# Optimization experiments

Hardware: AMD Instinct MI355X
Metric: run time of the kernel (lower is better)

The kernel has to match this reference:

```python
import jax, jax.numpy as jnp
import numpy as np

NUM_NODES = 512

def chebyshev_convolution(laplacian, signal, weights, t0):
    # Faithful port of the torch helper, including tk_prev staying equal to
    # `laplacian` throughout the loop (as in the source).
    k = weights.shape[0]
    # t0 is the identity, so t0 @ signal == signal
    out = jnp.matmul(signal, weights[0])
    out = out + jnp.matmul(jnp.matmul(laplacian, signal), weights[1])
    tk_prev = laplacian
    tk = 2.0 * jnp.matmul(laplacian, laplacian) - t0
    for i in range(2, k):
        out = out + jnp.matmul(jnp.matmul(tk, signal), weights[i])
        tk = 2.0 * jnp.matmul(laplacian, tk) - tk_prev
    return out


def setup_inputs() -> dict:
    key = jax.random.key(0)
    ks = jax.random.split(key, 5)
    B, T, N, C_IN, C_OUT, CS, CD = 4, 12, NUM_NODES, 64, 64, 3, 6
    std_l = 0.1 / np.sqrt(N)
    std_t = 0.1 / np.sqrt(C_IN)
    x = jax.random.normal(ks[0], (B, T, N, C_IN), dtype=jnp.float32)
    ws = jax.random.uniform(ks[1], (N, N), jnp.float32, -std_l, std_l)
    ts = jax.random.uniform(ks[2], (CS, C_IN, C_OUT), jnp.float32, -std_t, std_t)
    wp = jax.random.uniform(ks[3], (C_IN, C_IN), jnp.float32, -std_t, std_t)
    td = jax.random.uniform(ks[4], (CD, C_IN, C_OUT), jnp.float32, -std_t, std_t)
    return {"x": x, "ws": ws, "ts": ts, "wp": wp, "td": td}


def reference(x, ws, ts, wp, td):
    N = NUM_NODES
    t0 = jnp.eye(N, dtype=x.dtype)
    # Static (SGC) branch: Chebyshev conv with learned static Laplacian ws
    out_s = chebyshev_convolution(ws, x, ts, t0)
    # Dynamic branch: data-dependent Laplacian wd = x @ (wp @ x^T)  -> (B,T,N,N)
    wd = jnp.matmul(x, jnp.matmul(wp, jnp.swapaxes(x, -2, -1)))
    wd = wd + jnp.min(wd)
    wd = wd / jnp.max(wd) / (N ** 2)
    out_d = chebyshev_convolution(wd, x, td, t0)
    return out_s + out_d
```

## Files before the change

kernel.cpp:

```cpp
#include <hip/hip_runtime.h>
#include <cstddef>
#include <cstdint>

#define NN 512
#define CC 64
#define BT 48

typedef __bf16 bf16_t;
typedef bf16_t bf16x8 __attribute__((ext_vector_type(8)));
typedef bf16_t bf16x4 __attribute__((ext_vector_type(4)));
typedef float f32x4 __attribute__((ext_vector_type(4)));

#define OFF_MN    0
#define OFF_MX    384
#define OFF_WSB   1024
#define OFF_WS2B  132096
#define OFF_XBT   263168
#define OFF_XNB   1049600
#define OFF_XNR   1836032
#define OFF_CS0   2622464
#define OFF_T1T   2647040
#define OFF_T2T   2649088
#define OFF_Z1N   2651136
#define OFF_Z2N   3437568
#define OFF_WEB   4224000
#define OFF_WER   4322304
#define OFF_VDY   4420608

__device__ __forceinline__ f32x4 mfma(bf16x8 a, bf16x8 b, f32x4 c) {
  return __builtin_amdgcn_mfma_f32_16x16x32_bf16(a, b, c, 0, 0, 0);
}
__device__ __forceinline__ int swz_chunk(int r, int c8) {
  return r * 64 + ((c8 ^ (r & 7)) << 3);
}
__device__ __forceinline__ int swz_e(int r, int c) {
  return r * 64 + ((((c >> 3) ^ (r & 7)) << 3)) + (c & 7);
}
__device__ __forceinline__ bf16x8 frag(const bf16_t* sm, int row, int kc) {
  return *(const bf16x8*)(sm + row * 64 + ((kc ^ (row & 7)) << 3));
}
__device__ __forceinline__ void stage64(bf16_t* sm, const bf16_t* g, int ld, int tid) {
#pragma unroll
  for (int j = 0; j < 2; ++j) {
    int id = tid + 256 * j;
    int r = id >> 3, c8 = id & 7;
    bf16x8 v = *(const bf16x8*)(g + (size_t)r * ld + c8 * 8);
    *(bf16x8*)(sm + swz_chunk(r, c8)) = v;
  }
}
__device__ __forceinline__ void stage64f(bf16_t* sm, const float* g, int ld, int tid) {
#pragma unroll
  for (int j = 0; j < 4; ++j) {
    int idx = tid + 256 * j;
    int r = idx >> 4, cc = (idx & 15) * 4;
    float4 v = *(const float4*)(g + (size_t)r * ld + cc);
    bf16x4 o = {(bf16_t)v.x, (bf16_t)v.y, (bf16_t)v.z, (bf16_t)v.w};
    *(bf16x4*)(sm + swz_e(r, cc)) = o;
  }
}
struct bfpair { bf16_t b, r; };
__device__ __forceinline__ bfpair splitbf(float f) {
  bfpair p;
  p.b = (bf16_t)f;
  p.r = (bf16_t)(f - (float)p.b);
  return p;
}
__device__ __forceinline__ float dot16(const bf16_t* sm, int row, int sub,
                                       const float* vecF) {
  bf16x8 a0 = frag(sm, row, sub * 2);
  bf16x8 a1 = frag(sm, row, sub * 2 + 1);
  float s = 0.f;
#pragma unroll
  for (int q = 0; q < 8; ++q) {
    s += (float)a0[q] * vecF[sub * 16 + q];
    s += (float)a1[q] * vecF[sub * 16 + 8 + q];
  }
  return s;
}

__global__ __launch_bounds__(256) void k_pre(
    const float* __restrict__ x, const float* __restrict__ wsL,
    const float* __restrict__ ts, const float* __restrict__ wp,
    float* __restrict__ wsf)
{
  __shared__ __align__(16) char pool[32768];
  __shared__ float red[16];
  const int tid = threadIdx.x;
  const int b = blockIdx.x;
  const int w = tid >> 6, l = tid & 63, lh = l >> 4, lr = l & 15, m0 = w * 16;

  if (b < 384) {
    const int bt = (b & 7) + 8 * (b >> 6);
    const int it = (b >> 3) & 7;
    const int i0 = it * 64;
    float (*XsF)[66] = (float(*)[66])pool;
    bf16_t* XBT = (bf16_t*)(wsf + OFF_XBT);
    bf16_t* XNb = (bf16_t*)(wsf + OFF_XNB);
    bf16_t* XNr = (bf16_t*)(wsf + OFF_XNR);
    float* CS0 = wsf + OFF_CS0;
    const float* xg = x + ((size_t)bt * NN + i0) * CC;
    for (int j = 0; j < 4; ++j) {
      int idx = tid + 256 * j;
      int r = idx >> 4, c0v = (idx & 15) * 4;
      float4 v = *(const float4*)(xg + (size_t)r * CC + c0v);
      bfpair p0 = splitbf(v.x), p1 = splitbf(v.y), p2 = splitbf(v.z), p3 = splitbf(v.w);
      bf16x4 vb = {p0.b, p1.b, p2.b, p3.b};
      bf16x4 vr = {p0.r, p1.r, p2.r, p3.r};
      size_t gb = ((size_t)bt * 512 + i0 + r) * 64 + c0v;
      *(bf16x4*)(XNb + gb) = vb;
      *(bf16x4*)(XNr + gb) = vr;
      XsF[c0v + 0][r] = v.x; XsF[c0v + 1][r] = v.y;
      XsF[c0v + 2][r] = v.z; XsF[c0v + 3][r] = v.w;
    }
    __syncthreads();
    {
      int c = tid >> 2, k0 = (tid & 3) * 16;
      bf16x8 o1, o2;
#pragma unroll
      for (int q = 0; q < 8; ++q) {
        o1[q] = (bf16_t)XsF[c][k0 + q];
        o2[q] = (bf16_t)XsF[c][k0 + 8 + q];
      }
      size_t base = ((size_t)bt * 64 + c) * 512 + i0 + k0;
      *(bf16x8*)(XBT + base) = o1; *(bf16x8*)(XBT + base + 8) = o2;
    }
    if (tid < 64) {
      float s = 0.f;
      for (int r = 0; r < 64; ++r) s += XsF[tid][r];
      CS0[((size_t)bt * 8 + it) * 64 + tid] = s;
    }
    return;
  }
  if (b < 768) {
    const int g = b - 384;
    const int bt = (g & 7) + 8 * (g >> 6);
    const int bx = (g >> 3) & 7;
    bf16_t* WpT  = (bf16_t*)pool;
    bf16_t* Xa   = (bf16_t*)(pool + 8192);
    bf16_t* Hs   = (bf16_t*)(pool + 16384);
    bf16_t* Xcol = (bf16_t*)(pool + 24576);
    for (int j = 0; j < 4; ++j) {
      int idx = tid + 256 * j;
      int r = idx >> 4, cc = (idx & 15) * 4;
      float4 v = *(const float4*)(wp + r * 64 + cc);
      WpT[swz_e(cc + 0, r)] = (bf16_t)v.x;
      WpT[swz_e(cc + 1, r)] = (bf16_t)v.y;
      WpT[swz_e(cc + 2, r)] = (bf16_t)v.z;
      WpT[swz_e(cc + 3, r)] = (bf16_t)v.w;
    }
    stage64f(Xa, x + ((size_t)bt * NN + bx * 64) * CC, 64, tid);
    __syncthreads();
    f32x4 hacc[4] = {};
#pragma unroll
    for (int q = 0; q < 2; ++q) {
      bf16x8 a = frag(Xa, m0 + lr, q * 4 + lh);
#pragma unroll
      for (int t = 0; t < 4; ++t)
        hacc[t] = mfma(a, frag(WpT, t * 16 + lr, q * 4 + lh), hacc[t]);
    }
#pragma unroll
    for (int t = 0; t < 4; ++t)
#pragma unroll
      for (int r_ = 0; r_ < 4; ++r_)
        Hs[swz_e(m0 + 4 * lh + r_, t * 16 + lr)] = (bf16_t)hacc[t][r_];
    float mn = 3.4e38f, mx = -3.4e38f;
    for (int byj = 0; byj < 8; ++byj) {
      __syncthreads();
      stage64f(Xcol, x + ((size_t)bt * NN + byj * 64) * CC, 64, tid);
      __syncthreads();
      f32x4 acc[4] = {};
#pragma unroll
      for (int q = 0; q < 2; ++q) {
        bf16x8 a = frag(Hs, m0 + lr, q * 4 + lh);
#pragma unroll
        for (int t = 0; t < 4; ++t)
          acc[t] = mfma(a, frag(Xcol, t * 16 + lr, q * 4 + lh), acc[t]);
      }
#pragma unroll
      for (int t = 0; t < 4; ++t)
#pragma unroll
        for (int r_ = 0; r_ < 4; ++r_) {
          mn = fminf(mn, acc[t][r_]); mx = fmaxf(mx, acc[t][r_]);
        }
    }
    for (int off = 32; off; off >>= 1) {
      mn = fminf(mn, __shfl_xor(mn, off));
      mx = fmaxf(mx, __shfl_xor(mx, off));
    }
    if (l == 0) { red[w] = mn; red[8 + w] = mx; }
    __syncthreads();
    if (tid == 0) {
      mn = fminf(fminf(red[0], red[1]), fminf(red[2], red[3]));
      mx = fmaxf(fmaxf(red[8], red[9]), fmaxf(red[10], red[11]));
      wsf[OFF_MN + g] = mn; wsf[OFF_MX + g] = mx;
    }
    return;
  }
  if (b < 832) {
    const int idx2 = b - 768;
    bf16_t* Asb = (bf16_t*)pool;
    bf16_t* Bsb = (bf16_t*)(pool + 8192);
    bf16_t* Ys  = (bf16_t*)(pool + 16384);
    bf16_t* WS2B = (bf16_t*)(wsf + OFF_WS2B);
    const int r0 = (idx2 >> 3) * 64, c0 = (idx2 & 7) * 64;
    f32x4 acc[4] = {};
    for (int jj = 0; jj < 8; ++jj) {
      if (jj) __syncthreads();
      for (int j = 0; j < 4; ++j) {
        int idx = tid + 256 * j;
        int r = idx >> 4, cc = (idx & 15) * 4;
        float4 v = *(const float4*)(wsL + (size_t)(r0 + r) * 512 + jj * 64 + cc);
        bf16x4 vb = {(bf16_t)v.x, (bf16_t)v.y, (bf16_t)v.z, (bf16_t)v.w};
        *(bf16x4*)(Asb + swz_e(r, cc)) = vb;
        float4 u = *(const float4*)(wsL + (size_t)(jj * 64 + r) * 512 + c0 + cc);
        Bsb[swz_e(cc + 0, r)] = (bf16_t)u.x;
        Bsb[swz_e(cc + 1, r)] = (bf16_t)u.y;
        Bsb[swz_e(cc + 2, r)] = (bf16_t)u.z;
        Bsb[swz_e(cc + 3, r)] = (bf16_t)u.w;
      }
      __syncthreads();
#pragma unroll
      for (int q = 0; q < 2; ++q) {
        bf16x8 a = frag(Asb, m0 + lr, q * 4 + lh);
#pragma unroll
        for (int t = 0; t < 4; ++t)
          acc[t] = mfma(a, frag(Bsb, t * 16 + lr, q * 4 + lh), acc[t]);
      }
    }
#pragma unroll
    for (int t = 0; t < 4; ++t)
#pragma unroll
      for (int r_ = 0; r_ < 4; ++r_) {
        int row = m0 + 4 * lh + r_, col = t * 16 + lr;
        float v = 2.0f * acc[t][r_] - ((r0 + row) == (c0 + col) ? 1.0f : 0.0f);
        Ys[swz_e(row, col)] = (bf16_t)v;
      }
    __syncthreads();
#pragma unroll
    for (int j = 0; j < 2; ++j) {
      int id = tid + 256 * j;
      int r = id >> 3, c8 = id & 7;
      *(bf16x8*)(WS2B + (size_t)(r0 + r) * 512 + c0 + c8 * 8) =
          *(const bf16x8*)(Ys + swz_chunk(r, c8));
    }
    return;
  }
  if (b < 840) {
    const int bx = b - 832;
    const float* wrow = wsL + (size_t)bx * 64 * 512;
    bf16_t* wob = (bf16_t*)(wsf + OFF_WSB) + (size_t)bx * 64 * 512;
    for (int j = 0; j < 32; ++j) {
      int idx = tid + 256 * j;
      float4 v = *(const float4*)(wrow + (size_t)idx * 4);
      bf16x4 o = {(bf16_t)v.x, (bf16_t)v.y, (bf16_t)v.z, (bf16_t)v.w};
      *(bf16x4*)(wob + (size_t)idx * 4) = o;
    }
    return;
  }
  {
    bf16_t* T1 = (bf16_t*)(wsf + OFF_T1T);
    bf16_t* T2 = (bf16_t*)(wsf + OFF_T2T);
    const float* t1g = ts + 4096;
    const float* t2g = ts + 8192;
    for (int j = 0; j < 16; ++j) {
      int idx = tid + 256 * j;
      int cin = idx >> 6, co = idx & 63;
      T1[co * 64 + cin] = (bf16_t)t1g[cin * 64 + co];
      T2[co * 64 + cin] = (bf16_t)t2g[cin * 64 + co];
    }
  }
}

__global__ __launch_bounds__(256) void k_mix(
    const float* __restrict__ ts, const float* __restrict__ wp,
    const float* __restrict__ td, float* __restrict__ wsf)
{
  __shared__ __align__(16) char pool[66688];
  const int tid = threadIdx.x;
  const int bid = blockIdx.x;
  const int w = tid >> 6, l = tid & 63, lh = l >> 4, lr = l & 15, m0 = w * 16;

  if (bid >= 48) {
    const int g = bid - 48;
    const int bt = (g & 7) + 8 * (g >> 6);
    const int n0 = ((g >> 3) & 7) * 64;
    bf16_t* As = (bf16_t*)pool;
    bf16_t* B1 = (bf16_t*)(pool + 8192);
    bf16_t* B2 = (bf16_t*)(pool + 16384);
    const bf16_t* XBT = (const bf16_t*)(wsf + OFF_XBT);
    const bf16_t* WSB = (const bf16_t*)(wsf + OFF_WSB);
    const bf16_t* WS2B = (const bf16_t*)(wsf + OFF_WS2B);
    f32x4 acc1[4] = {}, acc2[4] = {};
    for (int kk = 0; kk < 8; ++kk) {
      if (kk) __syncthreads();
      stage64(As, XBT + (size_t)bt * 32768 + kk * 64, 512, tid);
      stage64(B1, WSB + (size_t)n0 * 512 + kk * 64, 512, tid);
      stage64(B2, WS2B + (size_t)n0 * 512 + kk * 64, 512, tid);
      __syncthreads();
#pragma unroll
      for (int q = 0; q < 2; ++q) {
        bf16x8 a = frag(As, m0 + lr, q * 4 + lh);
#pragma unroll
        for (int t = 0; t < 4; ++t) {
          acc1[t] = mfma(a, frag(B1, t * 16 + lr, q * 4 + lh), acc1[t]);
          acc2[t] = mfma(a, frag(B2, t * 16 + lr, q * 4 + lh), acc2[t]);
        }
      }
    }
    __syncthreads();
#pragma unroll
    for (int t = 0; t < 4; ++t)
#pragma unroll
      for (int r_ = 0; r_ < 4; ++r_) {
        int cy = m0 + 4 * lh + r_, nl = t * 16 + lr;
        As[swz_e(nl, cy)] = (bf16_t)acc1[t][r_];
        B1[swz_e(nl, cy)] = (bf16_t)acc2[t][r_];
      }
    __syncthreads();
    bf16_t* Z1N = (bf16_t*)(wsf + OFF_Z1N);
    bf16_t* Z2N = (bf16_t*)(wsf + OFF_Z2N);
#pragma unroll
    for (int j = 0; j < 2; ++j) {
      int id = tid + 256 * j;
      int r = id >> 3, c8 = id & 7;
      size_t gb = ((size_t)bt * 512 + n0 + r) * 64 + c8 * 8;
      *(bf16x8*)(Z1N + gb) = *(const bf16x8*)(As + swz_chunk(r, c8));
      *(bf16x8*)(Z2N + gb) = *(const bf16x8*)(B1 + swz_chunk(r, c8));
    }
    return;
  }
  const int bt = bid;
  bf16_t* XB  = (bf16_t*)pool;
  bf16_t* Ab0 = (bf16_t*)pool;
  bf16_t* AT0 = (bf16_t*)(pool + 8192);
  bf16_t* Ab1 = (bf16_t*)(pool + 16384);
  bf16_t* AT1 = (bf16_t*)(pool + 24576);
  bf16_t* Gb  = (bf16_t*)(pool + 32768);
  bf16_t* WpT = (bf16_t*)(pool + 40960);
  bf16_t* tdA = (bf16_t*)(pool + 49152);
  bf16_t* tdB = (bf16_t*)(pool + 57344);
  float* vec = (float*)(pool + 65536);
  float* uF = vec;        float* hF = vec + 64;
  float* b0 = vec + 128;  float* b1 = vec + 192;
  float* redv = vec + 256;
  const bf16_t* XBTg = (const bf16_t*)(wsf + OFF_XBT);
  const float* CS0 = wsf + OFF_CS0;
  for (int kk = 0; kk < 8; ++kk)
    stage64(XB + kk * 4096, XBTg + (size_t)bt * 32768 + kk * 64, 512, tid);
  {
    float mn = 3.4e38f, mx = -3.4e38f;
    for (int i = tid; i < 384; i += 256) {
      mn = fminf(mn, wsf[OFF_MN + i]);
      mx = fmaxf(mx, wsf[OFF_MX + i]);
    }
    for (int off = 32; off; off >>= 1) {
      mn = fminf(mn, __shfl_xor(mn, off));
      mx = fmaxf(mx, __shfl_xor(mx, off));
    }
    if (l == 0) { redv[w] = mn; redv[8 + w] = mx; }
  }
  if (tid < 64) {
    float s = 0.f;
#pragma unroll
    for (int p = 0; p < 8; ++p) s += CS0[((size_t)bt * 8 + p) * 64 + tid];
    uF[tid] = s; b0[tid] = s;
  }
  __syncthreads();
  f32x4 pacc[4] = {};
  for (int kk = 0; kk < 8; ++kk) {
    const bf16_t* xt = XB + kk * 4096;
#pragma unroll
    for (int q = 0; q < 2; ++q) {
      bf16x8 a = frag(xt, m0 + lr, q * 4 + lh);
#pragma unroll
      for (int t = 0; t < 4; ++t)
        pacc[t] = mfma(a, frag(xt, t * 16 + lr, q * 4 + lh), pacc[t]);
    }
  }
  const float mnA = fminf(fminf(redv[0], redv[1]), fminf(redv[2], redv[3]));
  const float mxA = fmaxf(fmaxf(redv[8], redv[9]), fmaxf(redv[10], redv[11]));
  const float s_sc = 1.0f / (mxA + mnA) / 262144.0f;
  const float c_sc = mnA * s_sc;
  __syncthreads();
#pragma unroll
  for (int t = 0; t < 4; ++t)
#pragma unroll
    for (int r_ = 0; r_ < 4; ++r_) {
      int m = m0 + 4 * lh + r_, jc = t * 16 + lr;
      bf16_t bv = (bf16_t)pacc[t][r_];
      Ab0[swz_e(m, jc)] = bv; AT0[swz_e(jc, m)] = bv;
    }
  for (int j = 0; j < 4; ++j) {
    int idx = tid + 256 * j;
    int r = idx >> 4, cc = (idx & 15) * 4;
    float4 v = *(const float4*)(wp + r * 64 + cc);
    WpT[swz_e(cc + 0, r)] = (bf16_t)v.x;
    WpT[swz_e(cc + 1, r)] = (bf16_t)v.y;
    WpT[swz_e(cc + 2, r)] = (bf16_t)v.z;
    WpT[swz_e(cc + 3, r)] = (bf16_t)v.w;
  }
  for (int j = 0; j < 4; ++j) {
    int idx = tid + 256 * j;
    int cin = idx >> 4, co = (idx & 15) * 4;
    float4 v = *(const float4*)(td + 4096 + cin * 64 + co);
    tdA[swz_e(co + 0, cin)] = (bf16_t)v.x;
    tdA[swz_e(co + 1, cin)] = (bf16_t)v.y;
    tdA[swz_e(co + 2, cin)] = (bf16_t)v.z;
    tdA[swz_e(co + 3, cin)] = (bf16_t)v.w;
  }
  __syncthreads();
  {
    int jj = tid >> 2, sub = tid & 3;
    float s = dot16(WpT, jj, sub, uF);
    s += __shfl_xor(s, 1); s += __shfl_xor(s, 2);
    if (sub == 0) hF[jj] = s;
  }
  {
    f32x4 gv[4] = {};
#pragma unroll
    for (int q = 0; q < 2; ++q) {
      bf16x8 a = frag(Ab0, m0 + lr, q * 4 + lh);
#pragma unroll
      for (int t = 0; t < 4; ++t)
        gv[t] = mfma(a, frag(WpT, t * 16 + lr, q * 4 + lh), gv[t]);
    }
#pragma unroll
    for (int t = 0; t < 4; ++t)
#pragma unroll
      for (int r_ = 0; r_ < 4; ++r_)
        Gb[swz_e(m0 + 4 * lh + r_, t * 16 + lr)] = (bf16_t)gv[t][r_];
  }
  __syncthreads();
  float mu = 0.f, vacc = 0.f;
  f32x4 Macc[4] = {};
  for (int i = 1; i <= 5; ++i) {
    const float* bcur = (i & 1) ? b0 : b1;
    float* bnx = (i & 1) ? b1 : b0;
    const bf16_t* tdc = (i & 1) ? tdA : tdB;
    const bf16_t* AbC = (i & 1) ? Ab0 : Ab1;
    const bf16_t* ATC = (i & 1) ? AT0 : AT1;
    bf16_t* AbN = (i & 1) ? Ab1 : Ab0;
    bf16_t* ATN = (i & 1) ? AT1 : AT0;
    if (i < 5) {
      bf16_t* tdn = (i & 1) ? tdB : tdA;
      for (int j = 0; j < 4; ++j) {
        int idx = tid + 256 * j;
        int cin = idx >> 4, co = (idx & 15) * 4;
        float4 v = *(const float4*)(td + (i + 1) * 4096 + cin * 64 + co);
        tdn[swz_e(co + 0, cin)] = (bf16_t)v.x;
        tdn[swz_e(co + 1, cin)] = (bf16_t)v.y;
        tdn[swz_e(co + 2, cin)] = (bf16_t)v.z;
        tdn[swz_e(co + 3, cin)] = (bf16_t)v.w;
      }
    }
#pragma unroll
    for (int q = 0; q < 2; ++q) {
      bf16x8 a = frag(AbC, m0 + lr, q * 4 + lh);
#pragma unroll
      for (int t = 0; t < 4; ++t)
        Macc[t] = mfma(a, frag(tdc, t * 16 + lr, q * 4 + lh), Macc[t]);
    }
    f32x4 Aacc[4] = {};
    if (i < 5) {
#pragma unroll
      for (int q = 0; q < 2; ++q) {
        bf16x8 gfr = frag(Gb, m0 + lr, q * 4 + lh);
#pragma unroll
        for (int t = 0; t < 4; ++t)
          Aacc[t] = mfma(gfr, frag(ATC, t * 16 + lr, q * 4 + lh), Aacc[t]);
      }
    }
    {
      int co = tid >> 2, sub = tid & 3;
      float sv = dot16(tdc, co, sub, bcur);
      sv += __shfl_xor(sv, 1); sv += __shfl_xor(sv, 2);
      if (sub == 0) vacc += sv;
    }
    if (i < 5) {
      int jj = tid >> 2, sub = tid & 3;
      float t1 = dot16(ATC, jj, sub, hF);
      t1 += __shfl_xor(t1, 1); t1 += __shfl_xor(t1, 2);
      if (sub == 0)
        bnx[jj] = 2.f * (s_sc * t1 + 512.f * c_sc * bcur[jj] + mu * uF[jj])
                  - (i >= 2 ? uF[jj] : 0.f);
    }
    if (i < 5) {
#pragma unroll
      for (int t = 0; t < 4; ++t)
#pragma unroll
        for (int r_ = 0; r_ < 4; ++r_) {
          int m = m0 + 4 * lh + r_, jc = t * 16 + lr;
          float v = 2.f * (s_sc * Aacc[t][r_] + c_sc * uF[m] * bcur[jc] + mu * pacc[t][r_])
                    - (i >= 2 ? pacc[t][r_] : 0.f);
          bf16_t bv = (bf16_t)v;
          AbN[swz_e(m, jc)] = bv; ATN[swz_e(jc, m)] = bv;
        }
      mu = (i == 1) ? -1.f : 0.f;
    }
    __syncthreads();
  }
  bf16_t* Mst = tdA;
  bf16_t* WpN = tdB;
#pragma unroll
  for (int t = 0; t < 4; ++t)
#pragma unroll
    for (int r_ = 0; r_ < 4; ++r_)
      Mst[swz_e(t * 16 + lr, m0 + 4 * lh + r_)] = (bf16_t)Macc[t][r_];
  for (int j = 0; j < 4; ++j) {
    int idx = tid + 256 * j;
    int r = idx >> 4, cc = (idx & 15) * 4;
    float4 v = *(const float4*)(wp + r * 64 + cc);
    bf16x4 o = {(bf16_t)v.x, (bf16_t)v.y, (bf16_t)v.z, (bf16_t)v.w};
    *(bf16x4*)(WpN + swz_e(r, cc)) = o;
  }
  __syncthreads();
  f32x4 wm[4] = {};
#pragma unroll
  for (int q = 0; q < 2; ++q) {
    bf16x8 a = frag(WpN, m0 + lr, q * 4 + lh);
#pragma unroll
    for (int t = 0; t < 4; ++t)
      wm[t] = mfma(a, frag(Mst, t * 16 + lr, q * 4 + lh), wm[t]);
  }
  bf16_t* WEb = (bf16_t*)(wsf + OFF_WEB);
  bf16_t* WEr = (bf16_t*)(wsf + OFF_WER);
#pragma unroll
  for (int t = 0; t < 4; ++t)
#pragma unroll
    for (int r_ = 0; r_ < 4; ++r_) {
      int a_ = m0 + 4 * lh + r_, co = t * 16 + lr;
      float weff = ts[a_ * 64 + co] + td[a_ * 64 + co] - td[2 * 4096 + a_ * 64 + co]
                   + s_sc * wm[t][r_];
      bfpair p = splitbf(weff);
      WEb[((size_t)bt * 64 + co) * 64 + a_] = p.b;
      WEr[((size_t)bt * 64 + co) * 64 + a_] = p.r;
    }
  if ((tid & 3) == 0) (wsf + OFF_VDY)[bt * 64 + (tid >> 2)] = c_sc * vacc;
}

__global__ __launch_bounds__(256) void k_epi(float* __restrict__ wsf,
                                             float* __restrict__ out)
{
  __shared__ __align__(16) bf16_t Xb[4096], Xr[4096], Z1s[4096], Z2s[4096],
                                  WEs[4096], WRs[4096], T1s[4096], T2s[4096];
  const int tid = threadIdx.x;
  const int g = blockIdx.x;
  const int bt = (g & 7) + 8 * (g >> 6);
  const int n0 = ((g >> 3) & 7) * 64;
  const int w = tid >> 6, l = tid & 63, lh = l >> 4, lr = l & 15, m0 = w * 16;
  stage64(Xb,  (const bf16_t*)(wsf + OFF_XNB) + ((size_t)bt * 512 + n0) * 64, 64, tid);
  stage64(Xr,  (const bf16_t*)(wsf + OFF_XNR) + ((size_t)bt * 512 + n0) * 64, 64, tid);
  stage64(Z1s, (const bf16_t*)(wsf + OFF_Z1N) + ((size_t)bt * 512 + n0) * 64, 64, tid);
  stage64(Z2s, (const bf16_t*)(wsf + OFF_Z2N) + ((size_t)bt * 512 + n0) * 64, 64, tid);
  stage64(WEs, (const bf16_t*)(wsf + OFF_WEB) + (size_t)bt * 4096, 64, tid);
  stage64(WRs, (const bf16_t*)(wsf + OFF_WER) + (size_t)bt * 4096, 64, tid);
  stage64(T1s, (const bf16_t*)(wsf + OFF_T1T), 64, tid);
  stage64(T2s, (const bf16_t*)(wsf + OFF_T2T), 64, tid);
  __syncthreads();
  const float* VDY = wsf + OFF_VDY;
  f32x4 accO[4];
#pragma unroll
  for (int t = 0; t < 4; ++t) {
    float vv = VDY[bt * 64 + t * 16 + lr];
    accO[t] = {vv, vv, vv, vv};
  }
#pragma unroll
  for (int q = 0; q < 2; ++q) {
    bf16x8 aXb = frag(Xb, m0 + lr, q * 4 + lh);
    bf16x8 aXr = frag(Xr, m0 + lr, q * 4 + lh);
    bf16x8 aZ1 = frag(Z1s, m0 + lr, q * 4 + lh);
    bf16x8 aZ2 = frag(Z2s, m0 + lr, q * 4 + lh);
#pragma unroll
    for (int t = 0; t < 4; ++t) {
      bf16x8 bWb = frag(WEs, t * 16 + lr, q * 4 + lh);
      bf16x8 bWr = frag(WRs, t * 16 + lr, q * 4 + lh);
      accO[t] = mfma(aXb, bWb, accO[t]);
      accO[t] = mfma(aXb, bWr, accO[t]);
      accO[t] = mfma(aXr, bWb, accO[t]);
      accO[t] = mfma(aZ1, frag(T1s, t * 16 + lr, q * 4 + lh), accO[t]);
      accO[t] = mfma(aZ2, frag(T2s, t * 16 + lr, q * 4 + lh), accO[t]);
    }
  }
#pragma unroll
  for (int t = 0; t < 4; ++t)
#pragma unroll
    for (int r_ = 0; r_ < 4; ++r_)
      out[((size_t)bt * 512 + n0 + m0 + 4 * lh + r_) * 64 + t * 16 + lr] = accO[t][r_];
}

extern "C" void kernel_launch(void* const* d_in, const int* in_sizes, int n_in,
                              void* d_out, int out_size, void* d_ws, size_t ws_size,
                              hipStream_t stream)
{
  (void)in_sizes; (void)n_in; (void)out_size; (void)ws_size;
  const float* x   = (const float*)d_in[0];
  const float* wsL = (const float*)d_in[1];
  const float* ts  = (const float*)d_in[2];
  const float* wp  = (const float*)d_in[3];
  const float* td  = (const float*)d_in[4];
  float* out = (float*)d_out;
  float* wsf = (float*)d_ws;
  dim3 b(256);

  k_pre<<<841, b, 0, stream>>>(x, wsL, ts, wp, wsf);
  k_mix<<<432, b, 0, stream>>>(ts, wp, td, wsf);
  k_epi<<<384, b, 0, stream>>>(wsf, out);
}
```

Before: 43.47 us.

## Split dynamic min/max blocks in half and shrink k_mix shared memory

Measured after the change: 44.98 us. +3.5%, slower.

```diff
diff --git a/kernel.cpp b/kernel.cpp
--- a/kernel.cpp
+++ b/kernel.cpp
@@ -12,20 +12,20 @@
 typedef float f32x4 __attribute__((ext_vector_type(4)));
 
 #define OFF_MN    0
-#define OFF_MX    384
-#define OFF_WSB   1024
-#define OFF_WS2B  132096
-#define OFF_XBT   263168
-#define OFF_XNB   1049600
-#define OFF_XNR   1836032
-#define OFF_CS0   2622464
-#define OFF_T1T   2647040
-#define OFF_T2T   2649088
-#define OFF_Z1N   2651136
-#define OFF_Z2N   3437568
-#define OFF_WEB   4224000
-#define OFF_WER   4322304
-#define OFF_VDY   4420608
+#define OFF_MX    768
+#define OFF_WSB   2048
+#define OFF_WS2B  133120
+#define OFF_XBT   264192
+#define OFF_XNB   1050624
+#define OFF_XNR   1837056
+#define OFF_CS0   2623488
+#define OFF_T1T   2648064
+#define OFF_T2T   2650112
+#define OFF_Z1N   2652160
+#define OFF_Z2N   3438592
+#define OFF_WEB   4225024
+#define OFF_WER   4323328
+#define OFF_VDY   4421632
 
 __device__ __forceinline__ f32x4 mfma(bf16x8 a, bf16x8 b, f32x4 c) {
   return __builtin_amdgcn_mfma_f32_16x16x32_bf16(a, b, c, 0, 0, 0);
@@ -131,10 +131,12 @@
     }
     return;
   }
-  if (b < 768) {
+  if (b < 1152) {
     const int g = b - 384;
-    const int bt = (g & 7) + 8 * (g >> 6);
-    const int bx = (g >> 3) & 7;
+    const int gg = (g >= 384) ? g - 384 : g;
+    const int half = (g >= 384) ? 1 : 0;
+    const int bt = (gg & 7) + 8 * (gg >> 6);
+    const int bx = (gg >> 3) & 7;
     bf16_t* WpT  = (bf16_t*)pool;
     bf16_t* Xa   = (bf16_t*)(pool + 8192);
     bf16_t* Hs   = (bf16_t*)(pool + 16384);
@@ -164,7 +166,7 @@
       for (int r_ = 0; r_ < 4; ++r_)
         Hs[swz_e(m0 + 4 * lh + r_, t * 16 + lr)] = (bf16_t)hacc[t][r_];
     float mn = 3.4e38f, mx = -3.4e38f;
-    for (int byj = 0; byj < 8; ++byj) {
+    for (int byj = half * 4; byj < half * 4 + 4; ++byj) {
       __syncthreads();
       stage64f(Xcol, x + ((size_t)bt * NN + byj * 64) * CC, 64, tid);
       __syncthreads();
@@ -196,8 +198,8 @@
     }
     return;
   }
-  if (b < 832) {
-    const int idx2 = b - 768;
+  if (b < 1216) {
+    const int idx2 = b - 1152;
     bf16_t* Asb = (bf16_t*)pool;
     bf16_t* Bsb = (bf16_t*)(pool + 8192);
     bf16_t* Ys  = (bf16_t*)(pool + 16384);
@@ -245,8 +247,8 @@
     }
     return;
   }
-  if (b < 840) {
-    const int bx = b - 832;
+  if (b < 1224) {
+    const int bx = b - 1216;
     const float* wrow = wsL + (size_t)bx * 64 * 512;
     bf16_t* wob = (bf16_t*)(wsf + OFF_WSB) + (size_t)bx * 64 * 512;
     for (int j = 0; j < 32; ++j) {
@@ -275,7 +277,7 @@
     const float* __restrict__ ts, const float* __restrict__ wp,
     const float* __restrict__ td, float* __restrict__ wsf)
 {
-  __shared__ __align__(16) char pool[66688];
+  __shared__ __align__(16) char pool[50240];
   const int tid = threadIdx.x;
   const int bid = blockIdx.x;
   const int w = tid >> 6, l = tid & 63, lh = l >> 4, lr = l & 15, m0 = w * 16;
@@ -330,51 +332,53 @@
     return;
   }
   const int bt = bid;
-  bf16_t* XB  = (bf16_t*)pool;
-  bf16_t* Ab0 = (bf16_t*)pool;
-  bf16_t* AT0 = (bf16_t*)(pool + 8192);
-  bf16_t* Ab1 = (bf16_t*)(pool + 16384);
-  bf16_t* AT1 = (bf16_t*)(pool + 24576);
-  bf16_t* Gb  = (bf16_t*)(pool + 32768);
-  bf16_t* WpT = (bf16_t*)(pool + 40960);
-  bf16_t* tdA = (bf16_t*)(pool + 49152);
-  bf16_t* tdB = (bf16_t*)(pool + 57344);
-  float* vec = (float*)(pool + 65536);
+  bf16_t* XB   = (bf16_t*)pool;
+  bf16_t* Ab0  = (bf16_t*)pool;
+  bf16_t* AT0  = (bf16_t*)(pool + 8192);
+  bf16_t* Ab1  = (bf16_t*)(pool + 16384);
+  bf16_t* AT1  = (bf16_t*)(pool + 24576);
+  bf16_t* Gb   = (bf16_t*)(pool + 32768);
+  bf16_t* WpTD = (bf16_t*)(pool + 40960);
+  float* vec = (float*)(pool + 49152);
   float* uF = vec;        float* hF = vec + 64;
   float* b0 = vec + 128;  float* b1 = vec + 192;
   float* redv = vec + 256;
   const bf16_t* XBTg = (const bf16_t*)(wsf + OFF_XBT);
   const float* CS0 = wsf + OFF_CS0;
-  for (int kk = 0; kk < 8; ++kk)
-    stage64(XB + kk * 4096, XBTg + (size_t)bt * 32768 + kk * 64, 512, tid);
-  {
-    float mn = 3.4e38f, mx = -3.4e38f;
-    for (int i = tid; i < 384; i += 256) {
-      mn = fminf(mn, wsf[OFF_MN + i]);
-      mx = fmaxf(mx, wsf[OFF_MX + i]);
-    }
-    for (int off = 32; off; off >>= 1) {
-      mn = fminf(mn, __shfl_xor(mn, off));
-      mx = fmaxf(mx, __shfl_xor(mx, off));
-    }
-    if (l == 0) { redv[w] = mn; redv[8 + w] = mx; }
-  }
-  if (tid < 64) {
-    float s = 0.f;
-#pragma unroll
-    for (int p = 0; p < 8; ++p) s += CS0[((size_t)bt * 8 + p) * 64 + tid];
-    uF[tid] = s; b0[tid] = s;
-  }
-  __syncthreads();
   f32x4 pacc[4] = {};
-  for (int kk = 0; kk < 8; ++kk) {
-    const bf16_t* xt = XB + kk * 4096;
-#pragma unroll
-    for (int q = 0; q < 2; ++q) {
-      bf16x8 a = frag(xt, m0 + lr, q * 4 + lh);
-#pragma unroll
-      for (int t = 0; t < 4; ++t)
-        pacc[t] = mfma(a, frag(xt, t * 16 + lr, q * 4 + lh), pacc[t]);
+  for (int pass = 0; pass < 2; ++pass) {
+    if (pass) __syncthreads();
+    for (int kk = 0; kk < 4; ++kk)
+      stage64(XB + kk * 4096,
+              XBTg + (size_t)bt * 32768 + (pass * 4 + kk) * 64, 512, tid);
+    if (pass == 0) {
+      float mn = 3.4e38f, mx = -3.4e38f;
+      for (int i = tid; i < 768; i += 256) {
+        mn = fminf(mn, wsf[OFF_MN + i]);
+        mx = fmaxf(mx, wsf[OFF_MX + i]);
+      }
+      for (int off = 32; off; off >>= 1) {
+        mn = fminf(mn, __shfl_xor(mn, off));
+        mx = fmaxf(mx, __shfl_xor(mx, off));
+      }
+      if (l == 0) { redv[w] = mn; redv[8 + w] = mx; }
+      if (tid < 64) {
+        float s = 0.f;
+#pragma unroll
+        for (int p = 0; p < 8; ++p) s += CS0[((size_t)bt * 8 + p) * 64 + tid];
+        uF[tid] = s; b0[tid] = s;
+      }
+    }
+    __syncthreads();
+    for (int kk = 0; kk < 4; ++kk) {
+      const bf16_t* xt = XB + kk * 4096;
+#pragma unroll
+      for (int q = 0; q < 2; ++q) {
+        bf16x8 a = frag(xt, m0 + lr, q * 4 + lh);
+#pragma unroll
+        for (int t = 0; t < 4; ++t)
+          pacc[t] = mfma(a, frag(xt, t * 16 + lr, q * 4 + lh), pacc[t]);
+      }
     }
   }
   const float mnA = fminf(fminf(redv[0], redv[1]), fminf(redv[2], redv[3]));
@@ -394,41 +398,42 @@
     int idx = tid + 256 * j;
     int r = idx >> 4, cc = (idx & 15) * 4;
     float4 v = *(const float4*)(wp + r * 64 + cc);
-    WpT[swz_e(cc + 0, r)] = (bf16_t)v.x;
-    WpT[swz_e(cc + 1, r)] = (bf16_t)v.y;
-    WpT[swz_e(cc + 2, r)] = (bf16_t)v.z;
-    WpT[swz_e(cc + 3, r)] = (bf16_t)v.w;
-  }
+    WpTD[swz_e(cc + 0, r)] = (bf16_t)v.x;
+    WpTD[swz_e(cc + 1, r)] = (bf16_t)v.y;
+    WpTD[swz_e(cc + 2, r)] = (bf16_t)v.z;
+    WpTD[swz_e(cc + 3, r)] = (bf16_t)v.w;
+  }
+  __syncthreads();
+  {
+    int jj = tid >> 2, sub = tid & 3;
+    float s = dot16(WpTD, jj, sub, uF);
+    s += __shfl_xor(s, 1); s += __shfl_xor(s, 2);
+    if (sub == 0) hF[jj] = s;
+  }
+  {
+    f32x4 gv[4] = {};
+#pragma unroll
+    for (int q = 0; q < 2; ++q) {
+      bf16x8 a = frag(Ab0, m0 + lr, q * 4 + lh);
+#pragma unroll
+      for (int t = 0; t < 4; ++t)
+        gv[t] = mfma(a, frag(WpTD, t * 16 + lr, q * 4 + lh), gv[t]);
+    }
+#pragma unroll
+    for (int t = 0; t < 4; ++t)
+#pragma unroll
+      for (int r_ = 0; r_ < 4; ++r_)
+        Gb[swz_e(m0 + 4 * lh + r_, t * 16 + lr)] = (bf16_t)gv[t][r_];
+  }
+  __syncthreads();
   for (int j = 0; j < 4; ++j) {
     int idx = tid + 256 * j;
     int cin = idx >> 4, co = (idx & 15) * 4;
     float4 v = *(const float4*)(td + 4096 + cin * 64 + co);
-    tdA[swz_e(co + 0, cin)] = (bf16_t)v.x;
-    tdA[swz_e(co + 1, cin)] = (bf16_t)v.y;
-    tdA[swz_e(co + 2, cin)] = (bf16_t)v.z;
-    tdA[swz_e(co + 3, cin)] = (bf16_t)v.w;
-  }
-  __syncthreads();
-  {
-    int jj = tid >> 2, sub = tid & 3;
-    float s = dot16(WpT, jj, sub, uF);
-    s += __shfl_xor(s, 1); s += __shfl_xor(s, 2);
-    if (sub == 0) hF[jj] = s;
-  }
-  {
-    f32x4 gv[4] = {};
-#pragma unroll
-    for (int q = 0; q < 2; ++q) {
-      bf16x8 a = frag(Ab0, m0 + lr, q * 4 + lh);
-#pragma unroll
-      for (int t = 0; t < 4; ++t)
-        gv[t] = mfma(a, frag(WpT, t * 16 + lr, q * 4 + lh), gv[t]);
-    }
-#pragma unroll
-    for (int t = 0; t < 4; ++t)
-#pragma unroll
-      for (int r_ = 0; r_ < 4; ++r_)
-        Gb[swz_e(m0 + 4 * lh + r_, t * 16 + lr)] = (bf16_t)gv[t][r_];
+    WpTD[swz_e(co + 0, cin)] = (bf16_t)v.x;
+    WpTD[swz_e(co + 1, cin)] = (bf16_t)v.y;
+    WpTD[swz_e(co + 2, cin)] = (bf16_t)v.z;
+    WpTD[swz_e(co + 3, cin)] = (bf16_t)v.w;
   }
   __syncthreads();
   float mu = 0.f, vacc = 0.f;
@@ -436,29 +441,16 @@
   for (int i = 1; i <= 5; ++i) {
     const float* bcur = (i & 1) ? b0 : b1;
     float* bnx = (i & 1) ? b1 : b0;
-    const bf16_t* tdc = (i & 1) ? tdA : tdB;
     const bf16_t* AbC = (i & 1) ? Ab0 : Ab1;
     const bf16_t* ATC = (i & 1) ? AT0 : AT1;
     bf16_t* AbN = (i & 1) ? Ab1 : Ab0;
     bf16_t* ATN = (i & 1) ? AT1 : AT0;
-    if (i < 5) {
-      bf16_t* tdn = (i & 1) ? tdB : tdA;
-      for (int j = 0; j < 4; ++j) {
-        int idx = tid + 256 * j;
-        int cin = idx >> 4, co = (idx & 15) * 4;
-        float4 v = *(const float4*)(td + (i + 1) * 4096 + cin * 64 + co);
-        tdn[swz_e(co + 0, cin)] = (bf16_t)v.x;
-        tdn[swz_e(co + 1, cin)] = (bf16_t)v.y;
-        tdn[swz_e(co + 2, cin)] = (bf16_t)v.z;
-        tdn[swz_e(co + 3, cin)] = (bf16_t)v.w;
-      }
-    }
 #pragma unroll
     for (int q = 0; q < 2; ++q) {
       bf16x8 a = frag(AbC, m0 + lr, q * 4 + lh);
 #pragma unroll
       for (int t = 0; t < 4; ++t)
-        Macc[t] = mfma(a, frag(tdc, t * 16 + lr, q * 4 + lh), Macc[t]);
+        Macc[t] = mfma(a, frag(WpTD, t * 16 + lr, q * 4 + lh), Macc[t]);
     }
     f32x4 Aacc[4] = {};
     if (i < 5) {
@@ -472,7 +464,7 @@
     }
     {
       int co = tid >> 2, sub = tid & 3;
-      float sv = dot16(tdc, co, sub, bcur);
+      float sv = dot16(WpTD, co, sub, bcur);
       sv += __shfl_xor(sv, 1); sv += __shfl_xor(sv, 2);
       if (sub == 0) vacc += sv;
     }
@@ -498,9 +490,21 @@
       mu = (i == 1) ? -1.f : 0.f;
     }
     __syncthreads();
-  }
-  bf16_t* Mst = tdA;
-  bf16_t* WpN = tdB;
+    if (i < 5) {
+      for (int j = 0; j < 4; ++j) {
+        int idx = tid + 256 * j;
+        int cin = idx >> 4, co = (idx & 15) * 4;
+        float4 v = *(const float4*)(td + (i + 1) * 4096 + cin * 64 + co);
+        WpTD[swz_e(co + 0, cin)] = (bf16_t)v.x;
+        WpTD[swz_e(co + 1, cin)] = (bf16_t)v.y;
+        WpTD[swz_e(co + 2, cin)] = (bf16_t)v.z;
+        WpTD[swz_e(co + 3, cin)] = (bf16_t)v.w;
+      }
+      __syncthreads();
+    }
+  }
+  bf16_t* Mst = Ab1;
+  bf16_t* WpN = AT1;
 #pragma unroll
   for (int t = 0; t < 4; ++t)
 #pragma unroll
@@ -602,7 +606,7 @@
   float* wsf = (float*)d_ws;
   dim3 b(256);
 
-  k_pre<<<841, b, 0, stream>>>(x, wsL, ts, wp, wsf);
-  k_mix<<<432, b, 0, stream>>>(ts, wp, td, wsf);
-  k_epi<<<384, b, 0, stream>>>(wsf, out);
-}
+  k_pre<<<1225, b, 0, stream>>>(x, wsL, ts, wp, wsf);
+  k_mix<<<432,  b, 0, stream>>>(ts, wp, td, wsf);
+  k_epi<<<384,  b, 0, stream>>>(wsf, out);
+}
```
